# Performance work log

Hardware: AMD Instinct MI355X
Metric: run time of the kernel (lower is better)

The kernel has to match this reference:

```python
import jax, jax.numpy as jnp
import numpy as np

BATCH, INPUT_DIM = 1024, 4096
LUT_SIZE, N_LUTS = 4, 16384
TABLE = 2 ** LUT_SIZE  # 16


def setup_inputs() -> dict:
    key = jax.random.key(0)
    k1, k2, k3, k4 = jax.random.split(key, 4)
    x = jax.random.uniform(k1, (BATCH, INPUT_DIM), dtype=jnp.float32)
    w = jax.random.normal(k2, (N_LUTS, TABLE), dtype=jnp.float32)
    w_comp = jax.random.normal(k3, (N_LUTS, TABLE), dtype=jnp.float32)
    indices = jax.random.randint(k4, (LUT_SIZE, N_LUTS), 0, INPUT_DIM, dtype=jnp.int32)
    return {"x": x, "w": w, "w_comp": w_comp, "indices": indices}


def get_probs(xr):
    # xr: [b, n, k] probabilities per LUT input
    x_ = jnp.stack([xr, 1.0 - xr], axis=-1)  # [b, n, k, 2]
    b, n, k, _ = x_.shape
    temp = x_[:, :, 0, :]  # [b, n, 2]
    for i in range(1, k):  # small fixed loop over lut_size-1 outer products
        temp = jnp.einsum('bnp,bnq->bnpq', temp, x_[:, :, i, :]).reshape(b, n, -1)
    # flip last dim, matching torch .flip(-1)
    return temp[..., ::-1]  # [b, n, 2**k]


def reference(x, w, w_comp, indices):
    # gather LUT inputs: indices is [k, n]; x[:, indices.T] -> [b, n, k]
    x_reordered = x[:, indices.T]
    logits = jnp.stack([w, w_comp], axis=0)          # [2, n, 2**k]
    sigma_w = jax.nn.softmax(logits, axis=0)[0]      # [n, 2**k]
    probs = get_probs(x_reordered)                   # [b, n, 2**k]
    return (probs * sigma_w).sum(-1)                 # [b, n]
```

## Files before the change

### kernel.cpp

```cpp
#include <hip/hip_runtime.h>

#define BATCH   1024
#define IDIM    4096
#define NLUTS   16384
#define TPB     256
#define NT      4
#define NPB     (TPB * NT)
#define NBLK_N  (NLUTS / NPB)
#define BTILE   16
#define NBLK_B  (BATCH / BTILE)
#define GRID    (NBLK_N * NBLK_B)

__global__ __launch_bounds__(TPB, 4)
void lut_fused(const float* __restrict__ x,
               const float* __restrict__ w,
               const float* __restrict__ wcomp,
               const int*   __restrict__ indices,
               float* __restrict__ out)
{
    __shared__ float xs[2][IDIM];

    int id    = blockIdx.x;
    int swz   = (id & 7) * (GRID / 8) + (id >> 3);
    int b_blk = swz / NBLK_N;
    int n_blk = swz % NBLK_N;

    int t  = threadIdx.x;
    int n0 = n_blk * NPB + t * NT;
    int b0 = b_blk * BTILE;

    int ix[NT][4];
#pragma unroll
    for (int i = 0; i < 4; ++i) {
        int4 v = *reinterpret_cast<const int4*>(indices + i * NLUTS + n0);
        ix[0][i] = v.x; ix[1][i] = v.y; ix[2][i] = v.z; ix[3][i] = v.w;
    }

    float a[NT][16];
#pragma unroll
    for (int q = 0; q < NT; ++q) {
        int n = n0 + q;
        float p[16];
#pragma unroll
        for (int k = 0; k < 4; ++k) {
            float4 wv = *reinterpret_cast<const float4*>(w     + (size_t)n * 16 + k * 4);
            float4 cv = *reinterpret_cast<const float4*>(wcomp + (size_t)n * 16 + k * 4);
            p[15 - (4 * k + 0)] = 1.f / (1.f + __expf(cv.x - wv.x));
            p[15 - (4 * k + 1)] = 1.f / (1.f + __expf(cv.y - wv.y));
            p[15 - (4 * k + 2)] = 1.f / (1.f + __expf(cv.z - wv.z));
            p[15 - (4 * k + 3)] = 1.f / (1.f + __expf(cv.w - wv.w));
        }
#pragma unroll
        for (int s = 8; s >= 1; s >>= 1) {
#pragma unroll
            for (int m = 0; m < 16; ++m) {
                if ((m & s) == 0) {
                    float t0 = p[m];
                    p[m]     = p[m + s];
                    p[m + s] = t0 - p[m + s];
                }
            }
        }
#pragma unroll
        for (int m = 0; m < 16; ++m) a[q][m] = p[m];
    }

    {
        const float* xrow = x + (size_t)b0 * IDIM;
#pragma unroll
        for (int k = 0; k < 4; ++k) {
            float4 r = *reinterpret_cast<const float4*>(xrow + (k * TPB + t) * 4);
            *reinterpret_cast<float4*>(&xs[0][(k * TPB + t) * 4]) = r;
        }
    }
    __syncthreads();

    for (int bi = 0; bi < BTILE; ++bi) {
        int  cur  = bi & 1;
        bool more = (bi + 1 < BTILE);

        float4 r[4];
        if (more) {
            const float* xrow = x + (size_t)(b0 + bi + 1) * IDIM;
#pragma unroll
            for (int k = 0; k < 4; ++k)
                r[k] = *reinterpret_cast<const float4*>(xrow + (k * TPB + t) * 4);
        }

        float res[NT];
#pragma unroll
        for (int q = 0; q < NT; ++q) {
            float xv0 = xs[cur][ix[q][0]];
            float xv1 = xs[cur][ix[q][1]];
            float xv2 = xs[cur][ix[q][2]];
            float xv3 = xs[cur][ix[q][3]];
            float h0 = fmaf(xv3, a[q][1],  a[q][0]);
            float h1 = fmaf(xv3, a[q][3],  a[q][2]);
            float h2 = fmaf(xv3, a[q][5],  a[q][4]);
            float h3 = fmaf(xv3, a[q][7],  a[q][6]);
            float h4 = fmaf(xv3, a[q][9],  a[q][8]);
            float h5 = fmaf(xv3, a[q][11], a[q][10]);
            float h6 = fmaf(xv3, a[q][13], a[q][12]);
            float h7 = fmaf(xv3, a[q][15], a[q][14]);
            float g0 = fmaf(xv2, h1, h0);
            float g1 = fmaf(xv2, h3, h2);
            float g2 = fmaf(xv2, h5, h4);
            float g3 = fmaf(xv2, h7, h6);
            float f0 = fmaf(xv1, g1, g0);
            float f1 = fmaf(xv1, g3, g2);
            res[q] = fmaf(xv0, f1, f0);
        }

        float4 o;
        o.x = res[0]; o.y = res[1]; o.z = res[2]; o.w = res[3];
        *reinterpret_cast<float4*>(out + (size_t)(b0 + bi) * NLUTS + n0) = o;

        if (more) {
            int nxt = cur ^ 1;
#pragma unroll
            for (int k = 0; k < 4; ++k)
                *reinterpret_cast<float4*>(&xs[nxt][(k * TPB + t) * 4]) = r[k];
        }
        __syncthreads();
    }
}

extern "C" void kernel_launch(void* const* d_in, const int* in_sizes, int n_in,
                              void* d_out, int out_size, void* d_ws, size_t ws_size,
                              hipStream_t stream) {
    const float* x   = (const float*)d_in[0];
    const float* w   = (const float*)d_in[1];
    const float* wc  = (const float*)d_in[2];
    const int*   idx = (const int*)d_in[3];
    float*       out = (float*)d_out;

    lut_fused<<<dim3(GRID), dim3(TPB), 0, stream>>>(x, w, wc, idx, out);
}
```

Measured before the change: 44.54 us.

## Precompute LUT coefficients in separate kernel and stage x via global_load_lds

Splits the per-LUT sigmoid and Möbius coefficient transform into a separate pre-kernel that writes to workspace. The main kernel reads those coefficients, uses 512-thread blocks that each cover 8 batch rows in groups of 2, and copies x rows straight into LDS with global_load_lds, interleaved so one float2 read returns both rows. It also remaps blocks to XCDs by batch. The aim is to stop recomputing the coefficients in every batch tile and to cut LDS and global traffic per output; the cost is an extra launch, a workspace round trip, and more coefficient reloads per block because each block covers fewer rows. The old fused kernel is kept as a fallback when the workspace is too small.

```diff
diff --git a/kernel.cpp b/kernel.cpp
--- a/kernel.cpp
+++ b/kernel.cpp
@@ -1,33 +1,71 @@
 #include <hip/hip_runtime.h>
+#include <stdint.h>
 
 #define BATCH   1024
 #define IDIM    4096
 #define NLUTS   16384
-#define TPB     256
+
+#define TPB     512
 #define NT      4
 #define NPB     (TPB * NT)
 #define NBLK_N  (NLUTS / NPB)
-#define BTILE   16
-#define NBLK_B  (BATCH / BTILE)
+#define BT      2
+#define G       4
+#define ROWS    (BT * G)
+#define NBLK_B  (BATCH / ROWS)
 #define GRID    (NBLK_N * NBLK_B)
 
+typedef __attribute__((address_space(3))) uint32_t lds_u32;
+typedef __attribute__((address_space(1))) uint32_t gbl_u32;
+
+__global__ void coeff_kernel(const float* __restrict__ w,
+                             const float* __restrict__ wc,
+                             float* __restrict__ cf)
+{
+    int n = blockIdx.x * 64 + threadIdx.x;
+    float p[16];
+#pragma unroll
+    for (int k = 0; k < 4; ++k) {
+        float4 wv = *reinterpret_cast<const float4*>(w  + (size_t)n * 16 + 4 * k);
+        float4 cv = *reinterpret_cast<const float4*>(wc + (size_t)n * 16 + 4 * k);
+        p[15 - (4 * k + 0)] = 1.f / (1.f + __expf(cv.x - wv.x));
+        p[15 - (4 * k + 1)] = 1.f / (1.f + __expf(cv.y - wv.y));
+        p[15 - (4 * k + 2)] = 1.f / (1.f + __expf(cv.z - wv.z));
+        p[15 - (4 * k + 3)] = 1.f / (1.f + __expf(cv.w - wv.w));
+    }
+#pragma unroll
+    for (int s = 8; s >= 1; s >>= 1) {
+#pragma unroll
+        for (int m = 0; m < 16; ++m) {
+            if ((m & s) == 0) { float t0 = p[m]; p[m] = p[m + s]; p[m + s] = t0 - p[m + s]; }
+        }
+    }
+#pragma unroll
+    for (int k = 0; k < 4; ++k) {
+        float4 o; o.x = p[4*k]; o.y = p[4*k+1]; o.z = p[4*k+2]; o.w = p[4*k+3];
+        *reinterpret_cast<float4*>(cf + (size_t)n * 16 + 4 * k) = o;
+    }
+}
+
 __global__ __launch_bounds__(TPB, 4)
-void lut_fused(const float* __restrict__ x,
-               const float* __restrict__ w,
-               const float* __restrict__ wcomp,
-               const int*   __restrict__ indices,
-               float* __restrict__ out)
+void lut_main(const float* __restrict__ x,
+              const float* __restrict__ cf,
+              const int*   __restrict__ indices,
+              float* __restrict__ out)
 {
-    __shared__ float xs[2][IDIM];
+    __shared__ float xs[2][IDIM * BT];
 
     int id    = blockIdx.x;
-    int swz   = (id & 7) * (GRID / 8) + (id >> 3);
-    int b_blk = swz / NBLK_N;
-    int n_blk = swz % NBLK_N;
+    int xcd   = id & 7;
+    int local = id >> 3;
+    int b_blk = xcd * 16 + (local & 15);
+    int n_blk = local >> 4;
 
     int t  = threadIdx.x;
+    int wv = t >> 6;
+    int ln = t & 63;
     int n0 = n_blk * NPB + t * NT;
-    int b0 = b_blk * BTILE;
+    int b0 = b_blk * ROWS;
 
     int ix[NT][4];
 #pragma unroll
@@ -39,87 +77,158 @@
     float a[NT][16];
 #pragma unroll
     for (int q = 0; q < NT; ++q) {
-        int n = n0 + q;
-        float p[16];
+#pragma unroll
+        for (int k = 0; k < 4; ++k) {
+            float4 v = *reinterpret_cast<const float4*>(cf + (size_t)(n0 + q) * 16 + 4 * k);
+            a[q][4*k] = v.x; a[q][4*k+1] = v.y; a[q][4*k+2] = v.z; a[q][4*k+3] = v.w;
+        }
+    }
+
+    int colbase = wv * 512 + (ln >> 1);
+    int par     = ln & 1;
+
+    auto stage = [&](int buf, int g) {
+        const float* src = x + (size_t)(b0 + g * BT + par) * IDIM + colbase;
+        float*       dst = &xs[buf][wv * 1024];
+#pragma unroll
+        for (int h = 0; h < 16; ++h) {
+            __builtin_amdgcn_global_load_lds((const gbl_u32*)(src + h * 32),
+                                             (lds_u32*)(dst + h * 64), 4, 0, 0);
+        }
+    };
+
+    stage(0, 0);
+    __syncthreads();
+
+#pragma unroll
+    for (int g = 0; g < G; ++g) {
+        int cur = g & 1;
+        if (g + 1 < G) stage(cur ^ 1, g + 1);
+
+        float res[NT][BT];
+#pragma unroll
+        for (int q = 0; q < NT; ++q) {
+            float2 xv0 = *reinterpret_cast<const float2*>(&xs[cur][ix[q][0] * 2]);
+            float2 xv1 = *reinterpret_cast<const float2*>(&xs[cur][ix[q][1] * 2]);
+            float2 xv2 = *reinterpret_cast<const float2*>(&xs[cur][ix[q][2] * 2]);
+            float2 xv3 = *reinterpret_cast<const float2*>(&xs[cur][ix[q][3] * 2]);
+#pragma unroll
+            for (int b = 0; b < BT; ++b) {
+                float v0 = b ? xv0.y : xv0.x;
+                float v1 = b ? xv1.y : xv1.x;
+                float v2 = b ? xv2.y : xv2.x;
+                float v3 = b ? xv3.y : xv3.x;
+                float h0 = fmaf(v3, a[q][1],  a[q][0]);
+                float h1 = fmaf(v3, a[q][3],  a[q][2]);
+                float h2 = fmaf(v3, a[q][5],  a[q][4]);
+                float h3 = fmaf(v3, a[q][7],  a[q][6]);
+                float h4 = fmaf(v3, a[q][9],  a[q][8]);
+                float h5 = fmaf(v3, a[q][11], a[q][10]);
+                float h6 = fmaf(v3, a[q][13], a[q][12]);
+                float h7 = fmaf(v3, a[q][15], a[q][14]);
+                float g0 = fmaf(v2, h1, h0);
+                float g1 = fmaf(v2, h3, h2);
+                float g2 = fmaf(v2, h5, h4);
+                float g3 = fmaf(v2, h7, h6);
+                float f0 = fmaf(v1, g1, g0);
+                float f1 = fmaf(v1, g3, g2);
+                res[q][b] = fmaf(v0, f1, f0);
+            }
+        }
+
+        size_t rbase = (size_t)(b0 + g * BT) * NLUTS + n0;
+        float4 o0; o0.x = res[0][0]; o0.y = res[1][0]; o0.z = res[2][0]; o0.w = res[3][0];
+        float4 o1; o1.x = res[0][1]; o1.y = res[1][1]; o1.z = res[2][1]; o1.w = res[3][1];
+        *reinterpret_cast<float4*>(out + rbase)         = o0;
+        *reinterpret_cast<float4*>(out + rbase + NLUTS) = o1;
+
+        __syncthreads();
+    }
+}
+
+#define F_TPB   256
+#define F_NT    4
+#define F_NPB   (F_TPB * F_NT)
+#define F_NBLKN (NLUTS / F_NPB)
+#define F_BTILE 16
+#define F_GRID  (F_NBLKN * (BATCH / F_BTILE))
+
+__global__ __launch_bounds__(F_TPB, 4)
+void lut_fused(const float* __restrict__ x, const float* __restrict__ w,
+               const float* __restrict__ wcomp, const int* __restrict__ indices,
+               float* __restrict__ out)
+{
+    __shared__ float xsf[2][IDIM];
+    int id = blockIdx.x;
+    int swz = (id & 7) * (F_GRID / 8) + (id >> 3);
+    int b_blk = swz / F_NBLKN, n_blk = swz % F_NBLKN;
+    int t = threadIdx.x;
+    int n0 = n_blk * F_NPB + t * F_NT;
+    int b0 = b_blk * F_BTILE;
+    int ix[F_NT][4];
+#pragma unroll
+    for (int i = 0; i < 4; ++i) {
+        int4 v = *reinterpret_cast<const int4*>(indices + i * NLUTS + n0);
+        ix[0][i] = v.x; ix[1][i] = v.y; ix[2][i] = v.z; ix[3][i] = v.w;
+    }
+    float a[F_NT][16];
+#pragma unroll
+    for (int q = 0; q < F_NT; ++q) {
+        int n = n0 + q; float p[16];
 #pragma unroll
         for (int k = 0; k < 4; ++k) {
             float4 wv = *reinterpret_cast<const float4*>(w     + (size_t)n * 16 + k * 4);
             float4 cv = *reinterpret_cast<const float4*>(wcomp + (size_t)n * 16 + k * 4);
-            p[15 - (4 * k + 0)] = 1.f / (1.f + __expf(cv.x - wv.x));
-            p[15 - (4 * k + 1)] = 1.f / (1.f + __expf(cv.y - wv.y));
-            p[15 - (4 * k + 2)] = 1.f / (1.f + __expf(cv.z - wv.z));
-            p[15 - (4 * k + 3)] = 1.f / (1.f + __expf(cv.w - wv.w));
-        }
-#pragma unroll
-        for (int s = 8; s >= 1; s >>= 1) {
-#pragma unroll
-            for (int m = 0; m < 16; ++m) {
-                if ((m & s) == 0) {
-                    float t0 = p[m];
-                    p[m]     = p[m + s];
-                    p[m + s] = t0 - p[m + s];
-                }
-            }
-        }
+            p[15-(4*k+0)] = 1.f/(1.f+__expf(cv.x-wv.x));
+            p[15-(4*k+1)] = 1.f/(1.f+__expf(cv.y-wv.y));
+            p[15-(4*k+2)] = 1.f/(1.f+__expf(cv.z-wv.z));
+            p[15-(4*k+3)] = 1.f/(1.f+__expf(cv.w-wv.w));
+        }
+#pragma unroll
+        for (int s = 8; s >= 1; s >>= 1)
+#pragma unroll
+            for (int m = 0; m < 16; ++m)
+                if ((m & s) == 0) { float t0 = p[m]; p[m] = p[m+s]; p[m+s] = t0 - p[m+s]; }
 #pragma unroll
         for (int m = 0; m < 16; ++m) a[q][m] = p[m];
     }
-
     {
         const float* xrow = x + (size_t)b0 * IDIM;
 #pragma unroll
-        for (int k = 0; k < 4; ++k) {
-            float4 r = *reinterpret_cast<const float4*>(xrow + (k * TPB + t) * 4);
-            *reinterpret_cast<float4*>(&xs[0][(k * TPB + t) * 4]) = r;
-        }
+        for (int k = 0; k < 4; ++k)
+            *reinterpret_cast<float4*>(&xsf[0][(k*F_TPB+t)*4]) =
+                *reinterpret_cast<const float4*>(xrow + (k*F_TPB+t)*4);
     }
     __syncthreads();
-
-    for (int bi = 0; bi < BTILE; ++bi) {
-        int  cur  = bi & 1;
-        bool more = (bi + 1 < BTILE);
-
+    for (int bi = 0; bi < F_BTILE; ++bi) {
+        int cur = bi & 1; bool more = (bi + 1 < F_BTILE);
         float4 r[4];
         if (more) {
-            const float* xrow = x + (size_t)(b0 + bi + 1) * IDIM;
+            const float* xrow = x + (size_t)(b0+bi+1) * IDIM;
 #pragma unroll
             for (int k = 0; k < 4; ++k)
-                r[k] = *reinterpret_cast<const float4*>(xrow + (k * TPB + t) * 4);
-        }
-
-        float res[NT];
-#pragma unroll
-        for (int q = 0; q < NT; ++q) {
-            float xv0 = xs[cur][ix[q][0]];
-            float xv1 = xs[cur][ix[q][1]];
-            float xv2 = xs[cur][ix[q][2]];
-            float xv3 = xs[cur][ix[q][3]];
-            float h0 = fmaf(xv3, a[q][1],  a[q][0]);
-            float h1 = fmaf(xv3, a[q][3],  a[q][2]);
-            float h2 = fmaf(xv3, a[q][5],  a[q][4]);
-            float h3 = fmaf(xv3, a[q][7],  a[q][6]);
-            float h4 = fmaf(xv3, a[q][9],  a[q][8]);
-            float h5 = fmaf(xv3, a[q][11], a[q][10]);
-            float h6 = fmaf(xv3, a[q][13], a[q][12]);
-            float h7 = fmaf(xv3, a[q][15], a[q][14]);
-            float g0 = fmaf(xv2, h1, h0);
-            float g1 = fmaf(xv2, h3, h2);
-            float g2 = fmaf(xv2, h5, h4);
-            float g3 = fmaf(xv2, h7, h6);
-            float f0 = fmaf(xv1, g1, g0);
-            float f1 = fmaf(xv1, g3, g2);
-            res[q] = fmaf(xv0, f1, f0);
-        }
-
-        float4 o;
-        o.x = res[0]; o.y = res[1]; o.z = res[2]; o.w = res[3];
-        *reinterpret_cast<float4*>(out + (size_t)(b0 + bi) * NLUTS + n0) = o;
-
+                r[k] = *reinterpret_cast<const float4*>(xrow + (k*F_TPB+t)*4);
+        }
+        float res[F_NT];
+#pragma unroll
+        for (int q = 0; q < F_NT; ++q) {
+            float v0 = xsf[cur][ix[q][0]], v1 = xsf[cur][ix[q][1]];
+            float v2 = xsf[cur][ix[q][2]], v3 = xsf[cur][ix[q][3]];
+            float h0 = fmaf(v3,a[q][1],a[q][0]),  h1 = fmaf(v3,a[q][3],a[q][2]);
+            float h2 = fmaf(v3,a[q][5],a[q][4]),  h3 = fmaf(v3,a[q][7],a[q][6]);
+            float h4 = fmaf(v3,a[q][9],a[q][8]),  h5 = fmaf(v3,a[q][11],a[q][10]);
+            float h6 = fmaf(v3,a[q][13],a[q][12]),h7 = fmaf(v3,a[q][15],a[q][14]);
+            float g0 = fmaf(v2,h1,h0), g1 = fmaf(v2,h3,h2);
+            float g2 = fmaf(v2,h5,h4), g3 = fmaf(v2,h7,h6);
+            res[q] = fmaf(v0, fmaf(v1,g3,g2), fmaf(v1,g1,g0));
+        }
+        float4 o; o.x=res[0]; o.y=res[1]; o.z=res[2]; o.w=res[3];
+        *reinterpret_cast<float4*>(out + (size_t)(b0+bi)*NLUTS + n0) = o;
         if (more) {
             int nxt = cur ^ 1;
 #pragma unroll
             for (int k = 0; k < 4; ++k)
-                *reinterpret_cast<float4*>(&xs[nxt][(k * TPB + t) * 4]) = r[k];
+                *reinterpret_cast<float4*>(&xsf[nxt][(k*F_TPB+t)*4]) = r[k];
         }
         __syncthreads();
     }
@@ -134,5 +243,11 @@
     const int*   idx = (const int*)d_in[3];
     float*       out = (float*)d_out;
 
-    lut_fused<<<dim3(GRID), dim3(TPB), 0, stream>>>(x, w, wc, idx, out);
-}
+    if (ws_size >= (size_t)NLUTS * 16 * sizeof(float)) {
+        float* cf = (float*)d_ws;
+        coeff_kernel<<<dim3(NLUTS / 64), dim3(64), 0, stream>>>(w, wc, cf);
+        lut_main<<<dim3(GRID), dim3(TPB), 0, stream>>>(x, cf, idx, out);
+    } else {
+        lut_fused<<<dim3(F_GRID), dim3(F_TPB), 0, stream>>>(x, w, wc, idx, out);
+    }
+}
```

Result: slower. 55.86 us (+25.4%).
